# Kernel optimization log

Hardware: AMD Instinct MI355X
Metric: run time of the kernel (lower is better)

## Reference

```python
import jax, jax.numpy as jnp
import numpy as np

B, S = 64, 128
NQ, C = 2000, 128
K, DE, DC = 64, 64, 64


def _glorot(k, shape):
    lim = float(np.sqrt(6.0 / (shape[0] + shape[1])))
    return jax.random.uniform(k, shape, jnp.float32, -lim, lim)


def setup_inputs() -> dict:
    key = jax.random.key(0)
    ks = jax.random.split(key, 16)
    return {
        'question_seq': jax.random.randint(ks[0], (B, S), 0, NQ, dtype=jnp.int32),
        'correctness_seq': jax.random.randint(ks[1], (B, S), 0, 2, dtype=jnp.int32),
        'q_matrix': (jax.random.uniform(ks[2], (NQ, C)) < 0.15).astype(jnp.float32),
        'E_q': jax.random.normal(ks[3], (NQ, DE), jnp.float32) * 0.02,
        'E_c': jax.random.normal(ks[4], (2, DC), jnp.float32) * 0.02,
        'h0': _glorot(ks[5], (C, K)),
        'W1': _glorot(ks[6], (DC + DE, K)), 'b1': jnp.zeros((K,), jnp.float32),
        'W2': _glorot(ks[7], (3 * K, K)), 'b2': jnp.zeros((K,), jnp.float32),
        'W3': _glorot(ks[8], (3 * K, K)), 'b3': jnp.zeros((K,), jnp.float32),
        'W4': _glorot(ks[9], (2 * K, K)), 'b4': jnp.zeros((K,), jnp.float32),
        'Wab': _glorot(ks[10], (K, 1)), 'bab': jnp.zeros((1,), jnp.float32),
        'Wdiff': _glorot(ks[11], (DE, C)), 'bdiff': jnp.zeros((C,), jnp.float32),
        'Wdisc': _glorot(ks[12], (DE, 1)), 'bdisc': jnp.zeros((1,), jnp.float32),
    }


def _forward(question_seq, correctness_seq, q_matrix, E_q, E_c, h0,
             W1, b1, W2, b2, W3, b3, W4, b4,
             Wab, bab, Wdiff, bdiff, Wdisc, bdisc):
    e_emb = E_q[question_seq]                 # [B,S,DE]
    c_emb = E_c[correctness_seq]              # [B,S,DC]
    all_learning = jnp.concatenate([e_emb, c_emb], -1) @ W1 + b1  # [B,S,K]
    q_seq = q_matrix[question_seq]            # [B,S,C]

    h_pre0 = jnp.broadcast_to(h0, (B, C, K))
    h_tilde0 = jnp.einsum('bc,ck->bk', q_seq[:, 0], h0)
    learning0 = jnp.zeros((B, K), jnp.float32)

    xs = (
        jnp.moveaxis(q_seq[:, :-1], 1, 0),        # q_e        [S-1,B,C]
        jnp.moveaxis(all_learning[:, :-1], 1, 0),  # learning   [S-1,B,K]
        jnp.moveaxis(q_seq[:, 1:], 1, 0),         # q_next     [S-1,B,C]
        jnp.moveaxis(e_emb[:, 1:], 1, 0),         # e_next     [S-1,B,DE]
    )

    def step(carry, x):
        h_pre, h_tilde_pre, learning_pre = carry
        q_e, learning, q_next, e_next = x
        cat = jnp.concatenate([learning_pre, learning, h_tilde_pre], -1)  # [B,3K]
        learning_gain = jnp.tanh(cat @ W2 + b2)
        gamma_l = jax.nn.sigmoid(cat @ W3 + b3)
        LG = gamma_l * (learning_gain + 1.0) * 0.5                       # [B,K]
        LG_tilde = q_e[:, :, None] * LG[:, None, :]                      # [B,C,K] rank-1 scatter
        gate_in = jnp.concatenate(
            [h_pre, jnp.broadcast_to(LG[:, None, :], (B, C, K))], -1)    # [B,C,2K]
        gamma_f = jax.nn.sigmoid(gate_in @ W4 + b4)
        h = LG_tilde + gamma_f * h_pre                                   # [B,C,K]
        ability = jax.nn.sigmoid(jnp.squeeze(h @ Wab + bab, -1)) * q_next  # [B,C]
        diff = jax.nn.sigmoid(e_next @ Wdiff + bdiff) * q_next             # [B,C]
        disc = jax.nn.sigmoid(e_next @ Wdisc + bdisc) * 5.0                # [B,1]
        y = jax.nn.sigmoid(jnp.sum(disc * (ability - diff), -1))          # [B]
        h_tilde = jnp.einsum('bc,bck->bk', q_next, h)
        return (h, h_tilde, learning), y

    _, ys = jax.lax.scan(step, (h_pre0, h_tilde0, learning0), xs)  # ys [S-1,B]
    pred = jnp.concatenate([jnp.zeros((B, 1), jnp.float32), ys.T], axis=1)  # [B,S]
    return pred


def reference(question_seq, correctness_seq, q_matrix, E_q, E_c, h0,
              W1, b1, W2, b2, W3, b3, W4, b4,
              Wab, bab, Wdiff, bdiff, Wdisc, bdisc):
    return _forward(question_seq, correctness_seq, q_matrix, E_q, E_c, h0,
                    W1, b1, W2, b2, W3, b3, W4, b4,
                    Wab, bab, Wdiff, bdiff, Wdisc, bdisc)
```

## Files before the change

### kernel.cpp

```cpp
#include <hip/hip_runtime.h>


constexpr int BB = 64, SS = 128, CD = 128;
constexpr int RECF = 136;
constexpr int HP2  = 72;

typedef short bf16x8 __attribute__((ext_vector_type(8)));
typedef float f32x4  __attribute__((ext_vector_type(4)));

#define BAR() asm volatile("s_waitcnt lgkmcnt(0)\ns_barrier" ::: "memory")

__device__ __forceinline__ short f2bf(float x) {
  unsigned u = __builtin_bit_cast(unsigned, x);
  unsigned r = u + 0x7fffu + ((u >> 16) & 1u);
  return (short)(r >> 16);
}
__device__ __forceinline__ unsigned pk2bf(float a, float b) {
  unsigned ua = __builtin_bit_cast(unsigned, a);
  unsigned ub = __builtin_bit_cast(unsigned, b);
  unsigned ra = ua + 0x7fffu + ((ua >> 16) & 1u);
  unsigned rb = ub + 0x7fffu + ((ub >> 16) & 1u);
  return (ra >> 16) | (rb & 0xffff0000u);
}
__device__ __forceinline__ float sigm(float x) {
  return __builtin_amdgcn_rcpf(1.f + __expf(-x));
}
__device__ __forceinline__ bf16x8 pack8(float4 a, float4 b) {
  uint4 u = {pk2bf(a.x, a.y), pk2bf(a.z, a.w), pk2bf(b.x, b.y), pk2bf(b.z, b.w)};
  return __builtin_bit_cast(bf16x8, u);
}
__device__ __forceinline__ void store_bf4(short* p, float a, float b, float c, float d) {
  uint2 v = {pk2bf(a, b), pk2bf(c, d)};
  *(uint2*)p = v;
}

__global__ void pcK(const float* __restrict__ W1, const float* __restrict__ W2,
                    const float* __restrict__ W3, const float* __restrict__ Ec,
                    const float* __restrict__ b1,
                    float* __restrict__ Kws, float* __restrict__ Uws) {
  int m = blockIdx.x, tid = threadIdx.x;
  if (m < 4) {
    const float* src = (m < 2 ? W2 : W3) + (m & 1) * 64 * 64;
    int k = tid & 63, dg = tid >> 6;
    float acc[16];
    #pragma unroll
    for (int i = 0; i < 16; ++i) acc[i] = 0.f;
    for (int j = 0; j < 64; ++j) {
      float w = src[j * 64 + k];
      #pragma unroll
      for (int i = 0; i < 16; ++i) acc[i] += W1[(dg * 16 + i) * 64 + j] * w;
    }
    #pragma unroll
    for (int i = 0; i < 16; ++i) Kws[m * 4096 + (dg * 16 + i) * 64 + k] = acc[i];
  } else {
    __shared__ float alc[2][64];
    if (tid < 128) {
      int cr = tid >> 6, k = tid & 63;
      float s = b1[k];
      for (int d = 0; d < 64; ++d) s += Ec[cr * 64 + d] * W1[(64 + d) * 64 + k];
      alc[cr][k] = s;
    }
    __syncthreads();
    if (tid < 128) {
      int cr = tid >> 6, k = tid & 63;
      float u2a = 0.f, u2b = 0.f, u3a = 0.f, u3b = 0.f;
      for (int j = 0; j < 64; ++j) {
        float a = alc[cr][j];
        u2a += a * W2[j * 64 + k];       u2b += a * W2[(64 + j) * 64 + k];
        u3a += a * W3[j * 64 + k];       u3b += a * W3[(64 + j) * 64 + k];
      }
      Uws[(0 + cr) * 64 + k] = u2a;  Uws[(2 + cr) * 64 + k] = u2b;
      Uws[(4 + cr) * 64 + k] = u3a;  Uws[(6 + cr) * 64 + k] = u3b;
    }
  }
}

__global__ void pcT(const float* __restrict__ Eq, const float* __restrict__ qmat,
                    const float* __restrict__ Wdiff, const float* __restrict__ bdiff,
                    const float* __restrict__ Wdisc, const float* __restrict__ bdisc,
                    const float* __restrict__ Kws,
                    float* __restrict__ T, float* __restrict__ DIFF, float* __restrict__ DISCq) {
  int q0 = blockIdx.x * 8, tid = threadIdx.x;
  __shared__ float e[8][64];
  for (int i = tid; i < 512; i += 256) e[i >> 6][i & 63] = Eq[(q0 + (i >> 6)) * 64 + (i & 63)];
  __syncthreads();
  {
    int m = tid >> 6, k = tid & 63;
    float acc[8] = {0.f, 0.f, 0.f, 0.f, 0.f, 0.f, 0.f, 0.f};
    for (int d = 0; d < 64; ++d) {
      float w = Kws[m * 4096 + d * 64 + k];
      #pragma unroll
      for (int qq = 0; qq < 8; ++qq) acc[qq] += e[qq][d] * w;
    }
    #pragma unroll
    for (int qq = 0; qq < 8; ++qq) T[(q0 + qq) * 256 + m * 64 + k] = acc[qq];
  }
  if (tid < 128) {
    int c = tid;
    float acc[8] = {0.f, 0.f, 0.f, 0.f, 0.f, 0.f, 0.f, 0.f};
    for (int d = 0; d < 64; ++d) {
      float w = Wdiff[d * 128 + c];
      #pragma unroll
      for (int qq = 0; qq < 8; ++qq) acc[qq] += e[qq][d] * w;
    }
    #pragma unroll
    for (int qq = 0; qq < 8; ++qq)
      DIFF[(q0 + qq) * 128 + c] = qmat[(q0 + qq) * 128 + c] * sigm(acc[qq] + bdiff[c]);
  } else if (tid < 136) {
    int qq = tid - 128;
    float s = 0.f;
    for (int d = 0; d < 64; ++d) s += e[qq][d] * Wdisc[d];
    DISCq[q0 + qq] = 5.f * sigm(s + bdisc[0]);
  }
}

__global__ void pcR(const int* __restrict__ qs, const int* __restrict__ cs,
                    const float* __restrict__ qmat,
                    const float* __restrict__ b2, const float* __restrict__ b3,
                    const float* __restrict__ T, const float* __restrict__ Uws,
                    float* __restrict__ REC) {
  int tid = threadIdx.x;
  for (int i = 0; i < 4; ++i) {
    int bs = blockIdx.x * 4 + i;
    int t  = bs & (SS - 1);
    int q_t = qs[bs];
    float* rec = REC + (size_t)bs * RECF;
    if (tid < 64) {
      int k = tid;
      float v2 = b2[k], v3 = b3[k];
      if (t >= 1) {
        int q1 = qs[bs - 1], c1 = cs[bs - 1];
        v2 += T[q1 * 256 + 64 + k]  + Uws[(2 + c1) * 64 + k];
        v3 += T[q1 * 256 + 192 + k] + Uws[(6 + c1) * 64 + k];
      }
      if (t >= 2) {
        int q2 = qs[bs - 2], c2 = cs[bs - 2];
        v2 += T[q2 * 256 + k]       + Uws[(0 + c2) * 64 + k];
        v3 += T[q2 * 256 + 128 + k] + Uws[(4 + c2) * 64 + k];
      }
      int pp = (k & 15) * 4 + (k >> 4);
      rec[pp] = v2; rec[64 + pp] = v3;
    }
    unsigned long long m = __ballot(qmat[q_t * 128 + tid] > 0.5f);
    int wv = tid >> 6, lane = tid & 63;
    if (lane == 0) {
      rec[128 + wv * 2]     = __uint_as_float((unsigned)m);
      rec[128 + wv * 2 + 1] = __uint_as_float((unsigned)(m >> 32));
    }
  }
}

__global__ void pcY(const int* __restrict__ qs, const float* __restrict__ qmat,
                    const float* __restrict__ DIFF, const float* __restrict__ DISCq,
                    const float* __restrict__ YP, const float* __restrict__ bab,
                    float* __restrict__ out) {
  int tid = threadIdx.x, lane = tid & 63, wv = tid >> 6;
  const float bab0 = bab[0];
  __shared__ float red[4][2];
  #pragma unroll
  for (int i = 0; i < 4; ++i) {
    int bs = blockIdx.x * 4 + i;
    int t  = bs & (SS - 1);
    float v = 0.f;
    if (t != 0) {
      int q_t = qs[bs];
      float yp = YP[(size_t)bs * 128 + tid];
      float qn = qmat[q_t * 128 + tid] > 0.5f ? 1.f : 0.f;
      v = sigm(yp + bab0) * qn - DIFF[q_t * 128 + tid];
    }
    v += __shfl_xor(v, 32); v += __shfl_xor(v, 16); v += __shfl_xor(v, 8);
    v += __shfl_xor(v, 4);  v += __shfl_xor(v, 2);  v += __shfl_xor(v, 1);
    if (lane == 0) red[i][wv] = v;
  }
  __syncthreads();
  if (tid < 4) {
    int bs = blockIdx.x * 4 + tid;
    int t  = bs & (SS - 1);
    if (t == 0) out[bs] = 0.f;
    else        out[bs] = sigm(DISCq[qs[bs]] * (red[tid][0] + red[tid][1]));
  }
}

__global__ __launch_bounds__(256, 1) __attribute__((amdgpu_waves_per_eu(1, 1)))
void lpkt_main(
    const float* __restrict__ h0,
    const float* __restrict__ W2, const float* __restrict__ W3,
    const float* __restrict__ W4, const float* __restrict__ b4,
    const float* __restrict__ Wab,
    const float* __restrict__ REC, float* __restrict__ YP) {
  __shared__ __align__(16) short hsb[CD * HP2];
  __shared__ __align__(16) short lgb[4 * 64];
  __shared__ __align__(16) float htbuf[3][64];

  const int b    = blockIdx.x;
  const int tid  = threadIdx.x;
  const int lane = tid & 63;
  const int wv   = tid >> 6;
  const int col  = lane & 15;
  const int quad = lane >> 4;
  const int bS   = b * SS;
  const f32x4 zz = {0.f, 0.f, 0.f, 0.f};

  const float* W4a = W4;
  const float* W4b = W4 + 64 * 64;
  const float* W2c = W2 + 128 * 64;
  const float* W3c = W3 + 128 * 64;

  bf16x8 bw4[4][2], bwb[4][2], bw2[4][2], bw3[4][2], bwab[2];
  float b4r[4];
  #pragma unroll
  for (int nb = 0; nb < 4; ++nb) {
    #pragma unroll
    for (int half = 0; half < 2; ++half)
      #pragma unroll
      for (int j = 0; j < 8; ++j) {
        int p  = half * 32 + quad * 8 + j;
        int ke = (p & 3) * 16 + (p >> 2);
        int kk = ke * 64 + nb * 16 + col;
        bw4[nb][half][j] = f2bf(W4a[kk]);
        bwb[nb][half][j] = f2bf(W4b[kk]);
        bw2[nb][half][j] = f2bf(W2c[kk]);
        bw3[nb][half][j] = f2bf(W3c[kk]);
      }
    b4r[nb] = b4[nb * 16 + col];
  }
  #pragma unroll
  for (int half = 0; half < 2; ++half)
    #pragma unroll
    for (int j = 0; j < 8; ++j) {
      int p  = half * 32 + quad * 8 + j;
      int ke = (p & 3) * 16 + (p >> 2);
      bwab[half][j] = (col == 0) ? f2bf(Wab[ke]) : (short)0;
    }

  float h2[2][4][4];
  #pragma unroll
  for (int mt = 0; mt < 2; ++mt)
    #pragma unroll
    for (int reg = 0; reg < 4; ++reg) {
      int c = 32 * wv + 16 * mt + 4 * quad + reg;
      #pragma unroll
      for (int n = 0; n < 4; ++n) h2[mt][reg][n] = h0[c * 64 + n * 16 + col];
      store_bf4(&hsb[c * HP2 + col * 4],
                h2[mt][reg][0], h2[mt][reg][1], h2[mt][reg][2], h2[mt][reg][3]);
    }
  if (tid < 192) htbuf[tid >> 6][tid & 63] = 0.f;
  __syncthreads();

  float qeR[2][4];
  {
    unsigned qw = __float_as_uint(REC[(size_t)bS * RECF + 128 + wv]);
    float pk[4] = {0.f, 0.f, 0.f, 0.f};
    #pragma unroll
    for (int mt = 0; mt < 2; ++mt) {
      #pragma unroll
      for (int reg = 0; reg < 4; ++reg)
        qeR[mt][reg] = (float)((qw >> (16 * mt + 4 * quad + reg)) & 1u);
      #pragma unroll
      for (int n = 0; n < 4; ++n)
        pk[n] += qeR[mt][0] * h2[mt][0][n] + qeR[mt][1] * h2[mt][1][n]
               + qeR[mt][2] * h2[mt][2][n] + qeR[mt][3] * h2[mt][3][n];
    }
    #pragma unroll
    for (int n = 0; n < 4; ++n) {
      pk[n] += __shfl_xor(pk[n], 16);
      pk[n] += __shfl_xor(pk[n], 32);
    }
    if (quad == 0) {
      #pragma unroll
      for (int n = 0; n < 4; ++n) atomicAdd(&htbuf[1][col * 4 + n], pk[n]);
    }
  }

  unsigned qbw[2];
  qbw[1] = __float_as_uint(REC[(size_t)(bS + 1) * RECF + 128 + wv]);
  qbw[0] = __float_as_uint(REC[(size_t)(bS + 2) * RECF + 128 + wv]);
  float4 pb2[2], pb3[2];
  pb2[1] = *(const float4*)&REC[(size_t)(bS + 1) * RECF + col * 4];
  pb3[1] = *(const float4*)&REC[(size_t)(bS + 1) * RECF + 64 + col * 4];
  pb2[0] = *(const float4*)&REC[(size_t)(bS + 2) * RECF + col * 4];
  pb3[0] = *(const float4*)&REC[(size_t)(bS + 2) * RECF + 64 + col * 4];
  BAR();

  float qnR[2][4];

  for (int t = 1; t < SS; ++t) {
    const float* htb = htbuf[t % 3];
    float4 x0 = *(const float4*)&htb[quad * 8];
    float4 x1 = *(const float4*)&htb[quad * 8 + 4];
    float4 x2 = *(const float4*)&htb[32 + quad * 8];
    float4 x3 = *(const float4*)&htb[32 + quad * 8 + 4];
    bf16x8 af[2][2];
    #pragma unroll
    for (int mt = 0; mt < 2; ++mt) {
      int r = 32 * wv + 16 * mt + col;
      af[mt][0] = *(const bf16x8*)&hsb[r * HP2 + quad * 8];
      af[mt][1] = *(const bf16x8*)&hsb[r * HP2 + 32 + quad * 8];
    }

    unsigned qw = qbw[t & 1];
    #pragma unroll
    for (int mt = 0; mt < 2; ++mt)
      #pragma unroll
      for (int reg = 0; reg < 4; ++reg)
        qnR[mt][reg] = (float)((qw >> (16 * mt + 4 * quad + reg)) & 1u);
    float4 base2 = pb2[t & 1], base3 = pb3[t & 1];
    {
      int tn = (t + 2 < SS) ? t + 2 : SS - 1;
      const float* rn = REC + (size_t)(bS + tn) * RECF;
      qbw[t & 1] = __float_as_uint(rn[128 + wv]);
      pb2[t & 1] = *(const float4*)&rn[col * 4];
      pb3[t & 1] = *(const float4*)&rn[64 + col * 4];
    }

    f32x4 acc[2][4];
    #pragma unroll
    for (int mt = 0; mt < 2; ++mt)
      #pragma unroll
      for (int nb = 0; nb < 4; ++nb) {
        acc[mt][nb] = __builtin_amdgcn_mfma_f32_16x16x32_bf16(af[mt][0], bw4[nb][0], zz, 0, 0, 0);
        acc[mt][nb] = __builtin_amdgcn_mfma_f32_16x16x32_bf16(af[mt][1], bw4[nb][1], acc[mt][nb], 0, 0, 0);
      }
    #pragma unroll
    for (int mt = 0; mt < 2; ++mt) {
      f32x4 ya = __builtin_amdgcn_mfma_f32_16x16x32_bf16(af[mt][0], bwab[0], zz, 0, 0, 0);
      ya = __builtin_amdgcn_mfma_f32_16x16x32_bf16(af[mt][1], bwab[1], ya, 0, 0, 0);
      if (col == 0)
        *(float4*)&YP[((size_t)bS + t - 1) * 128 + 32 * wv + 16 * mt + 4 * quad]
            = make_float4(ya[0], ya[1], ya[2], ya[3]);
    }

    bf16x8 hf0 = pack8(x0, x1), hf1 = pack8(x2, x3);
    float lg[4];
    #pragma unroll
    for (int nb = 0; nb < 4; ++nb) {
      f32x4 a2 = __builtin_amdgcn_mfma_f32_16x16x32_bf16(hf0, bw2[nb][0], zz, 0, 0, 0);
      a2 = __builtin_amdgcn_mfma_f32_16x16x32_bf16(hf1, bw2[nb][1], a2, 0, 0, 0);
      f32x4 a3 = __builtin_amdgcn_mfma_f32_16x16x32_bf16(hf0, bw3[nb][0], zz, 0, 0, 0);
      a3 = __builtin_amdgcn_mfma_f32_16x16x32_bf16(hf1, bw3[nb][1], a3, 0, 0, 0);
      float u2 = a2[0] + ((const float*)&base2)[nb];
      float u3 = a3[0] + ((const float*)&base3)[nb];
      lg[nb] = sigm(u3) * sigm(2.f * u2);
    }
    if (quad == 0) store_bf4(&lgb[wv * 64 + col * 4], lg[0], lg[1], lg[2], lg[3]);
    bf16x8 lf0 = *(const bf16x8*)&lgb[wv * 64 + quad * 8];
    bf16x8 lf1 = *(const bf16x8*)&lgb[wv * 64 + 32 + quad * 8];
    float tvv[4];
    #pragma unroll
    for (int nb = 0; nb < 4; ++nb) {
      f32x4 bb = __builtin_amdgcn_mfma_f32_16x16x32_bf16(lf0, bwb[nb][0], zz, 0, 0, 0);
      bb = __builtin_amdgcn_mfma_f32_16x16x32_bf16(lf1, bwb[nb][1], bb, 0, 0, 0);
      tvv[nb] = bb[0] + b4r[nb];
    }

    #pragma unroll
    for (int mt = 0; mt < 2; ++mt)
      #pragma unroll
      for (int reg = 0; reg < 4; ++reg) {
        int c = 32 * wv + 16 * mt + 4 * quad + reg;
        #pragma unroll
        for (int nb = 0; nb < 4; ++nb) {
          float g = sigm(acc[mt][nb][reg] + tvv[nb]);
          h2[mt][reg][nb] = qeR[mt][reg] * lg[nb] + g * h2[mt][reg][nb];
        }
        store_bf4(&hsb[c * HP2 + col * 4],
                  h2[mt][reg][0], h2[mt][reg][1], h2[mt][reg][2], h2[mt][reg][3]);
      }

    {
      float pk[4] = {0.f, 0.f, 0.f, 0.f};
      #pragma unroll
      for (int mt = 0; mt < 2; ++mt)
        #pragma unroll
        for (int nb = 0; nb < 4; ++nb)
          pk[nb] += qnR[mt][0] * h2[mt][0][nb] + qnR[mt][1] * h2[mt][1][nb]
                  + qnR[mt][2] * h2[mt][2][nb] + qnR[mt][3] * h2[mt][3][nb];
      #pragma unroll
      for (int nb = 0; nb < 4; ++nb) {
        pk[nb] += __shfl_xor(pk[nb], 16);
        pk[nb] += __shfl_xor(pk[nb], 32);
      }
      if (quad == 0) {
        float* dst = htbuf[(t + 1) % 3];
        #pragma unroll
        for (int nb = 0; nb < 4; ++nb) atomicAdd(&dst[col * 4 + nb], pk[nb]);
      }
    }
    if (wv == 3) htbuf[(t + 2) % 3][lane] = 0.f;
    #pragma unroll
    for (int mt = 0; mt < 2; ++mt)
      #pragma unroll
      for (int reg = 0; reg < 4; ++reg) qeR[mt][reg] = qnR[mt][reg];
    BAR();
  }

  #pragma unroll
  for (int mt = 0; mt < 2; ++mt) {
    int r = 32 * wv + 16 * mt + col;
    bf16x8 af0 = *(const bf16x8*)&hsb[r * HP2 + quad * 8];
    bf16x8 af1 = *(const bf16x8*)&hsb[r * HP2 + 32 + quad * 8];
    f32x4 ya = __builtin_amdgcn_mfma_f32_16x16x32_bf16(af0, bwab[0], zz, 0, 0, 0);
    ya = __builtin_amdgcn_mfma_f32_16x16x32_bf16(af1, bwab[1], ya, 0, 0, 0);
    if (col == 0)
      *(float4*)&YP[((size_t)bS + 127) * 128 + 32 * wv + 16 * mt + 4 * quad]
          = make_float4(ya[0], ya[1], ya[2], ya[3]);
  }
}

extern "C" void kernel_launch(void* const* d_in, const int* in_sizes, int n_in,
                              void* d_out, int out_size, void* d_ws, size_t ws_size,
                              hipStream_t stream) {
  const int*   qs    = (const int*)d_in[0];
  const int*   cs    = (const int*)d_in[1];
  const float* qmat  = (const float*)d_in[2];
  const float* Eq    = (const float*)d_in[3];
  const float* Ec    = (const float*)d_in[4];
  const float* h0    = (const float*)d_in[5];
  const float* W1    = (const float*)d_in[6];
  const float* b1    = (const float*)d_in[7];
  const float* W2    = (const float*)d_in[8];
  const float* b2    = (const float*)d_in[9];
  const float* W3    = (const float*)d_in[10];
  const float* b3    = (const float*)d_in[11];
  const float* W4    = (const float*)d_in[12];
  const float* b4    = (const float*)d_in[13];
  const float* Wab   = (const float*)d_in[14];
  const float* bab   = (const float*)d_in[15];
  const float* Wdiff = (const float*)d_in[16];
  const float* bdiff = (const float*)d_in[17];
  const float* Wdisc = (const float*)d_in[18];
  const float* bdisc = (const float*)d_in[19];
  float* out = (float*)d_out;

  float* w = (float*)d_ws;
  float* Kws   = w;
  float* Uws   = Kws + 16384;
  float* T     = Uws + 512;
  float* DIFF  = T + 512000;
  float* DISCq = DIFF + 256000;
  float* REC   = DISCq + 2000;
  float* YP    = REC + (size_t)BB * SS * RECF;

  pcK<<<5, 256, 0, stream>>>(W1, W2, W3, Ec, b1, Kws, Uws);
  pcT<<<250, 256, 0, stream>>>(Eq, qmat, Wdiff, bdiff, Wdisc, bdisc, Kws, T, DIFF, DISCq);
  pcR<<<BB * SS / 4, 128, 0, stream>>>(qs, cs, qmat, b2, b3, T, Uws, REC);
  lpkt_main<<<BB, 256, 0, stream>>>(h0, W2, W3, W4, b4, Wab, REC, YP);
  pcY<<<BB * SS / 4, 128, 0, stream>>>(qs, qmat, DIFF, DISCq, YP, bab, out);
}
```

Before: 429.5 us.

## Restructure recurrent step to compute per-wave partial projections and fold pcK into pcT

The main recurrent kernel now has each wave multiply its partial h_tilde by W2/W3 with MFMA right after the state update. The partials go into double-buffered shared memory and are summed at the start of the next step. This replaces the LDS atomicAdd reduction into a triple-buffered htbuf and moves the W4 gate matmul and ability readout to the end of the step, shortening the critical path between barriers. The small pcK launch is removed: pcT now computes the E_q·W1 product and then W2/W3 per question tile, with block 0 also computing the Uws terms. This saves one launch but repeats W1 work in every block, and the YP indexing is shifted to match the new step ordering.

```diff
diff --git a/kernel.cpp b/kernel.cpp
--- a/kernel.cpp
+++ b/kernel.cpp
@@ -25,34 +25,61 @@
 __device__ __forceinline__ float sigm(float x) {
   return __builtin_amdgcn_rcpf(1.f + __expf(-x));
 }
-__device__ __forceinline__ bf16x8 pack8(float4 a, float4 b) {
-  uint4 u = {pk2bf(a.x, a.y), pk2bf(a.z, a.w), pk2bf(b.x, b.y), pk2bf(b.z, b.w)};
-  return __builtin_bit_cast(bf16x8, u);
-}
 __device__ __forceinline__ void store_bf4(short* p, float a, float b, float c, float d) {
   uint2 v = {pk2bf(a, b), pk2bf(c, d)};
   *(uint2*)p = v;
 }
 
-__global__ void pcK(const float* __restrict__ W1, const float* __restrict__ W2,
+__global__ void pcT(const float* __restrict__ Eq, const float* __restrict__ qmat,
+                    const float* __restrict__ W1, const float* __restrict__ W2,
                     const float* __restrict__ W3, const float* __restrict__ Ec,
                     const float* __restrict__ b1,
-                    float* __restrict__ Kws, float* __restrict__ Uws) {
-  int m = blockIdx.x, tid = threadIdx.x;
-  if (m < 4) {
+                    const float* __restrict__ Wdiff, const float* __restrict__ bdiff,
+                    const float* __restrict__ Wdisc, const float* __restrict__ bdisc,
+                    float* __restrict__ T, float* __restrict__ DIFF,
+                    float* __restrict__ DISCq, float* __restrict__ Uws) {
+  int q0 = blockIdx.x * 8, tid = threadIdx.x;
+  __shared__ float e[8][64], al[8][64];
+  for (int i = tid; i < 512; i += 256) e[i >> 6][i & 63] = Eq[(q0 + (i >> 6)) * 64 + (i & 63)];
+  __syncthreads();
+  for (int i = tid; i < 512; i += 256) {
+    int qq = i >> 6, k = i & 63;
+    float s = 0.f;
+    #pragma unroll 8
+    for (int d = 0; d < 64; ++d) s += e[qq][d] * W1[d * 64 + k];
+    al[qq][k] = s;
+  }
+  __syncthreads();
+  {
+    int m = tid >> 6, k = tid & 63;
     const float* src = (m < 2 ? W2 : W3) + (m & 1) * 64 * 64;
-    int k = tid & 63, dg = tid >> 6;
-    float acc[16];
-    #pragma unroll
-    for (int i = 0; i < 16; ++i) acc[i] = 0.f;
+    float acc[8] = {0.f, 0.f, 0.f, 0.f, 0.f, 0.f, 0.f, 0.f};
     for (int j = 0; j < 64; ++j) {
       float w = src[j * 64 + k];
       #pragma unroll
-      for (int i = 0; i < 16; ++i) acc[i] += W1[(dg * 16 + i) * 64 + j] * w;
-    }
-    #pragma unroll
-    for (int i = 0; i < 16; ++i) Kws[m * 4096 + (dg * 16 + i) * 64 + k] = acc[i];
-  } else {
+      for (int qq = 0; qq < 8; ++qq) acc[qq] += al[qq][j] * w;
+    }
+    #pragma unroll
+    for (int qq = 0; qq < 8; ++qq) T[(q0 + qq) * 256 + m * 64 + k] = acc[qq];
+  }
+  if (tid < 128) {
+    int c = tid;
+    float acc[8] = {0.f, 0.f, 0.f, 0.f, 0.f, 0.f, 0.f, 0.f};
+    for (int d = 0; d < 64; ++d) {
+      float w = Wdiff[d * 128 + c];
+      #pragma unroll
+      for (int qq = 0; qq < 8; ++qq) acc[qq] += e[qq][d] * w;
+    }
+    #pragma unroll
+    for (int qq = 0; qq < 8; ++qq)
+      DIFF[(q0 + qq) * 128 + c] = qmat[(q0 + qq) * 128 + c] * sigm(acc[qq] + bdiff[c]);
+  } else if (tid < 136) {
+    int qq = tid - 128;
+    float s = 0.f;
+    for (int d = 0; d < 64; ++d) s += e[qq][d] * Wdisc[d];
+    DISCq[q0 + qq] = 5.f * sigm(s + bdisc[0]);
+  }
+  if (blockIdx.x == 0) {
     __shared__ float alc[2][64];
     if (tid < 128) {
       int cr = tid >> 6, k = tid & 63;
@@ -72,45 +99,6 @@
       Uws[(0 + cr) * 64 + k] = u2a;  Uws[(2 + cr) * 64 + k] = u2b;
       Uws[(4 + cr) * 64 + k] = u3a;  Uws[(6 + cr) * 64 + k] = u3b;
     }
-  }
-}
-
-__global__ void pcT(const float* __restrict__ Eq, const float* __restrict__ qmat,
-                    const float* __restrict__ Wdiff, const float* __restrict__ bdiff,
-                    const float* __restrict__ Wdisc, const float* __restrict__ bdisc,
-                    const float* __restrict__ Kws,
-                    float* __restrict__ T, float* __restrict__ DIFF, float* __restrict__ DISCq) {
-  int q0 = blockIdx.x * 8, tid = threadIdx.x;
-  __shared__ float e[8][64];
-  for (int i = tid; i < 512; i += 256) e[i >> 6][i & 63] = Eq[(q0 + (i >> 6)) * 64 + (i & 63)];
-  __syncthreads();
-  {
-    int m = tid >> 6, k = tid & 63;
-    float acc[8] = {0.f, 0.f, 0.f, 0.f, 0.f, 0.f, 0.f, 0.f};
-    for (int d = 0; d < 64; ++d) {
-      float w = Kws[m * 4096 + d * 64 + k];
-      #pragma unroll
-      for (int qq = 0; qq < 8; ++qq) acc[qq] += e[qq][d] * w;
-    }
-    #pragma unroll
-    for (int qq = 0; qq < 8; ++qq) T[(q0 + qq) * 256 + m * 64 + k] = acc[qq];
-  }
-  if (tid < 128) {
-    int c = tid;
-    float acc[8] = {0.f, 0.f, 0.f, 0.f, 0.f, 0.f, 0.f, 0.f};
-    for (int d = 0; d < 64; ++d) {
-      float w = Wdiff[d * 128 + c];
-      #pragma unroll
-      for (int qq = 0; qq < 8; ++qq) acc[qq] += e[qq][d] * w;
-    }
-    #pragma unroll
-    for (int qq = 0; qq < 8; ++qq)
-      DIFF[(q0 + qq) * 128 + c] = qmat[(q0 + qq) * 128 + c] * sigm(acc[qq] + bdiff[c]);
-  } else if (tid < 136) {
-    int qq = tid - 128;
-    float s = 0.f;
-    for (int d = 0; d < 64; ++d) s += e[qq][d] * Wdisc[d];
-    DISCq[q0 + qq] = 5.f * sigm(s + bdisc[0]);
   }
 }
 
@@ -190,7 +178,8 @@
     const float* __restrict__ REC, float* __restrict__ YP) {
   __shared__ __align__(16) short hsb[CD * HP2];
   __shared__ __align__(16) short lgb[4 * 64];
-  __shared__ __align__(16) float htbuf[3][64];
+  __shared__ __align__(16) short pkb[4 * 64];
+  __shared__ __align__(16) float up[2][4][2][64];
 
   const int b    = blockIdx.x;
   const int tid  = threadIdx.x;
@@ -244,33 +233,57 @@
       store_bf4(&hsb[c * HP2 + col * 4],
                 h2[mt][reg][0], h2[mt][reg][1], h2[mt][reg][2], h2[mt][reg][3]);
     }
-  if (tid < 192) htbuf[tid >> 6][tid & 63] = 0.f;
-  __syncthreads();
-
-  float qeR[2][4];
+
+  unsigned qe_w = __float_as_uint(REC[(size_t)bS * RECF + 128 + wv]);
   {
-    unsigned qw = __float_as_uint(REC[(size_t)bS * RECF + 128 + wv]);
     float pk[4] = {0.f, 0.f, 0.f, 0.f};
     #pragma unroll
-    for (int mt = 0; mt < 2; ++mt) {
-      #pragma unroll
-      for (int reg = 0; reg < 4; ++reg)
-        qeR[mt][reg] = (float)((qw >> (16 * mt + 4 * quad + reg)) & 1u);
-      #pragma unroll
-      for (int n = 0; n < 4; ++n)
-        pk[n] += qeR[mt][0] * h2[mt][0][n] + qeR[mt][1] * h2[mt][1][n]
-               + qeR[mt][2] * h2[mt][2][n] + qeR[mt][3] * h2[mt][3][n];
-    }
+    for (int mt = 0; mt < 2; ++mt)
+      #pragma unroll
+      for (int reg = 0; reg < 4; ++reg) {
+        float q = (float)((qe_w >> (16 * mt + 4 * quad + reg)) & 1u);
+        #pragma unroll
+        for (int n = 0; n < 4; ++n) pk[n] += q * h2[mt][reg][n];
+      }
     #pragma unroll
     for (int n = 0; n < 4; ++n) {
       pk[n] += __shfl_xor(pk[n], 16);
       pk[n] += __shfl_xor(pk[n], 32);
     }
+    if (quad == 0) store_bf4(&pkb[wv * 64 + col * 4], pk[0], pk[1], pk[2], pk[3]);
+  }
+  bf16x8 pf0 = *(const bf16x8*)&pkb[wv * 64 + quad * 8];
+  bf16x8 pf1 = *(const bf16x8*)&pkb[wv * 64 + 32 + quad * 8];
+  {
+    float v2[4], v3[4];
+    #pragma unroll
+    for (int nb = 0; nb < 4; ++nb) {
+      f32x4 a2 = __builtin_amdgcn_mfma_f32_16x16x32_bf16(pf0, bw2[nb][0], zz, 0, 0, 0);
+      a2 = __builtin_amdgcn_mfma_f32_16x16x32_bf16(pf1, bw2[nb][1], a2, 0, 0, 0);
+      f32x4 a3 = __builtin_amdgcn_mfma_f32_16x16x32_bf16(pf0, bw3[nb][0], zz, 0, 0, 0);
+      a3 = __builtin_amdgcn_mfma_f32_16x16x32_bf16(pf1, bw3[nb][1], a3, 0, 0, 0);
+      v2[nb] = a2[0]; v3[nb] = a3[0];
+    }
     if (quad == 0) {
-      #pragma unroll
-      for (int n = 0; n < 4; ++n) atomicAdd(&htbuf[1][col * 4 + n], pk[n]);
-    }
-  }
+      *(float4*)&up[1][wv][0][col * 4] = make_float4(v2[0], v2[1], v2[2], v2[3]);
+      *(float4*)&up[1][wv][1][col * 4] = make_float4(v3[0], v3[1], v3[2], v3[3]);
+    }
+  }
+  bf16x8 af[2][2];
+  #pragma unroll
+  for (int mt = 0; mt < 2; ++mt) {
+    int r = 32 * wv + 16 * mt + col;
+    af[mt][0] = *(const bf16x8*)&hsb[r * HP2 + quad * 8];
+    af[mt][1] = *(const bf16x8*)&hsb[r * HP2 + 32 + quad * 8];
+  }
+  f32x4 acc[2][4];
+  #pragma unroll
+  for (int mt = 0; mt < 2; ++mt)
+    #pragma unroll
+    for (int nb = 0; nb < 4; ++nb) {
+      acc[mt][nb] = __builtin_amdgcn_mfma_f32_16x16x32_bf16(af[mt][0], bw4[nb][0], zz, 0, 0, 0);
+      acc[mt][nb] = __builtin_amdgcn_mfma_f32_16x16x32_bf16(af[mt][1], bw4[nb][1], acc[mt][nb], 0, 0, 0);
+    }
 
   unsigned qbw[2];
   qbw[1] = __float_as_uint(REC[(size_t)(bS + 1) * RECF + 128 + wv]);
@@ -282,38 +295,100 @@
   pb3[0] = *(const float4*)&REC[(size_t)(bS + 2) * RECF + 64 + col * 4];
   BAR();
 
-  float qnR[2][4];
-
   for (int t = 1; t < SS; ++t) {
-    const float* htb = htbuf[t % 3];
-    float4 x0 = *(const float4*)&htb[quad * 8];
-    float4 x1 = *(const float4*)&htb[quad * 8 + 4];
-    float4 x2 = *(const float4*)&htb[32 + quad * 8];
-    float4 x3 = *(const float4*)&htb[32 + quad * 8 + 4];
-    bf16x8 af[2][2];
+    const int par = t & 1;
+    float4 u2v = pb2[par], u3v = pb3[par];
+    {
+      float4 a0 = *(const float4*)&up[par][0][0][col * 4];
+      float4 a1 = *(const float4*)&up[par][1][0][col * 4];
+      float4 a2 = *(const float4*)&up[par][2][0][col * 4];
+      float4 a3 = *(const float4*)&up[par][3][0][col * 4];
+      float4 c0 = *(const float4*)&up[par][0][1][col * 4];
+      float4 c1 = *(const float4*)&up[par][1][1][col * 4];
+      float4 c2 = *(const float4*)&up[par][2][1][col * 4];
+      float4 c3 = *(const float4*)&up[par][3][1][col * 4];
+      u2v.x += a0.x + a1.x + a2.x + a3.x;  u3v.x += c0.x + c1.x + c2.x + c3.x;
+      u2v.y += a0.y + a1.y + a2.y + a3.y;  u3v.y += c0.y + c1.y + c2.y + c3.y;
+      u2v.z += a0.z + a1.z + a2.z + a3.z;  u3v.z += c0.z + c1.z + c2.z + c3.z;
+      u2v.w += a0.w + a1.w + a2.w + a3.w;  u3v.w += c0.w + c1.w + c2.w + c3.w;
+    }
+    float lg[4];
+    lg[0] = sigm(u3v.x) * sigm(2.f * u2v.x);
+    lg[1] = sigm(u3v.y) * sigm(2.f * u2v.y);
+    lg[2] = sigm(u3v.z) * sigm(2.f * u2v.z);
+    lg[3] = sigm(u3v.w) * sigm(2.f * u2v.w);
+    if (quad == 0) store_bf4(&lgb[wv * 64 + col * 4], lg[0], lg[1], lg[2], lg[3]);
+    unsigned qn_w = qbw[par];
+    {
+      int tn = (t + 2 < SS) ? t + 2 : SS - 1;
+      const float* rn = REC + (size_t)(bS + tn) * RECF;
+      qbw[par] = __float_as_uint(rn[128 + wv]);
+      pb2[par] = *(const float4*)&rn[col * 4];
+      pb3[par] = *(const float4*)&rn[64 + col * 4];
+    }
+    bf16x8 lf0 = *(const bf16x8*)&lgb[wv * 64 + quad * 8];
+    bf16x8 lf1 = *(const bf16x8*)&lgb[wv * 64 + 32 + quad * 8];
+    float tvv[4];
+    #pragma unroll
+    for (int nb = 0; nb < 4; ++nb) {
+      f32x4 bb = __builtin_amdgcn_mfma_f32_16x16x32_bf16(lf0, bwb[nb][0], zz, 0, 0, 0);
+      bb = __builtin_amdgcn_mfma_f32_16x16x32_bf16(lf1, bwb[nb][1], bb, 0, 0, 0);
+      tvv[nb] = bb[0] + b4r[nb];
+    }
+    #pragma unroll
+    for (int mt = 0; mt < 2; ++mt)
+      #pragma unroll
+      for (int reg = 0; reg < 4; ++reg) {
+        int c = 32 * wv + 16 * mt + 4 * quad + reg;
+        float qe = (float)((qe_w >> (16 * mt + 4 * quad + reg)) & 1u);
+        #pragma unroll
+        for (int nb = 0; nb < 4; ++nb) {
+          float g = sigm(acc[mt][nb][reg] + tvv[nb]);
+          h2[mt][reg][nb] = qe * lg[nb] + g * h2[mt][reg][nb];
+        }
+        store_bf4(&hsb[c * HP2 + col * 4],
+                  h2[mt][reg][0], h2[mt][reg][1], h2[mt][reg][2], h2[mt][reg][3]);
+      }
+    {
+      float pk[4] = {0.f, 0.f, 0.f, 0.f};
+      #pragma unroll
+      for (int mt = 0; mt < 2; ++mt)
+        #pragma unroll
+        for (int reg = 0; reg < 4; ++reg) {
+          float q = (float)((qn_w >> (16 * mt + 4 * quad + reg)) & 1u);
+          #pragma unroll
+          for (int n = 0; n < 4; ++n) pk[n] += q * h2[mt][reg][n];
+        }
+      #pragma unroll
+      for (int n = 0; n < 4; ++n) {
+        pk[n] += __shfl_xor(pk[n], 16);
+        pk[n] += __shfl_xor(pk[n], 32);
+      }
+      if (quad == 0) store_bf4(&pkb[wv * 64 + col * 4], pk[0], pk[1], pk[2], pk[3]);
+    }
+    pf0 = *(const bf16x8*)&pkb[wv * 64 + quad * 8];
+    pf1 = *(const bf16x8*)&pkb[wv * 64 + 32 + quad * 8];
+    {
+      float v2[4], v3[4];
+      #pragma unroll
+      for (int nb = 0; nb < 4; ++nb) {
+        f32x4 a2 = __builtin_amdgcn_mfma_f32_16x16x32_bf16(pf0, bw2[nb][0], zz, 0, 0, 0);
+        a2 = __builtin_amdgcn_mfma_f32_16x16x32_bf16(pf1, bw2[nb][1], a2, 0, 0, 0);
+        f32x4 a3 = __builtin_amdgcn_mfma_f32_16x16x32_bf16(pf0, bw3[nb][0], zz, 0, 0, 0);
+        a3 = __builtin_amdgcn_mfma_f32_16x16x32_bf16(pf1, bw3[nb][1], a3, 0, 0, 0);
+        v2[nb] = a2[0]; v3[nb] = a3[0];
+      }
+      if (quad == 0) {
+        *(float4*)&up[par ^ 1][wv][0][col * 4] = make_float4(v2[0], v2[1], v2[2], v2[3]);
+        *(float4*)&up[par ^ 1][wv][1][col * 4] = make_float4(v3[0], v3[1], v3[2], v3[3]);
+      }
+    }
     #pragma unroll
     for (int mt = 0; mt < 2; ++mt) {
       int r = 32 * wv + 16 * mt + col;
       af[mt][0] = *(const bf16x8*)&hsb[r * HP2 + quad * 8];
       af[mt][1] = *(const bf16x8*)&hsb[r * HP2 + 32 + quad * 8];
     }
-
-    unsigned qw = qbw[t & 1];
-    #pragma unroll
-    for (int mt = 0; mt < 2; ++mt)
-      #pragma unroll
-      for (int reg = 0; reg < 4; ++reg)
-        qnR[mt][reg] = (float)((qw >> (16 * mt + 4 * quad + reg)) & 1u);
-    float4 base2 = pb2[t & 1], base3 = pb3[t & 1];
-    {
-      int tn = (t + 2 < SS) ? t + 2 : SS - 1;
-      const float* rn = REC + (size_t)(bS + tn) * RECF;
-      qbw[t & 1] = __float_as_uint(rn[128 + wv]);
-      pb2[t & 1] = *(const float4*)&rn[col * 4];
-      pb3[t & 1] = *(const float4*)&rn[64 + col * 4];
-    }
-
-    f32x4 acc[2][4];
     #pragma unroll
     for (int mt = 0; mt < 2; ++mt)
       #pragma unroll
@@ -326,84 +401,11 @@
       f32x4 ya = __builtin_amdgcn_mfma_f32_16x16x32_bf16(af[mt][0], bwab[0], zz, 0, 0, 0);
       ya = __builtin_amdgcn_mfma_f32_16x16x32_bf16(af[mt][1], bwab[1], ya, 0, 0, 0);
       if (col == 0)
-        *(float4*)&YP[((size_t)bS + t - 1) * 128 + 32 * wv + 16 * mt + 4 * quad]
+        *(float4*)&YP[((size_t)bS + t) * 128 + 32 * wv + 16 * mt + 4 * quad]
             = make_float4(ya[0], ya[1], ya[2], ya[3]);
     }
-
-    bf16x8 hf0 = pack8(x0, x1), hf1 = pack8(x2, x3);
-    float lg[4];
-    #pragma unroll
-    for (int nb = 0; nb < 4; ++nb) {
-      f32x4 a2 = __builtin_amdgcn_mfma_f32_16x16x32_bf16(hf0, bw2[nb][0], zz, 0, 0, 0);
-      a2 = __builtin_amdgcn_mfma_f32_16x16x32_bf16(hf1, bw2[nb][1], a2, 0, 0, 0);
-      f32x4 a3 = __builtin_amdgcn_mfma_f32_16x16x32_bf16(hf0, bw3[nb][0], zz, 0, 0, 0);
-      a3 = __builtin_amdgcn_mfma_f32_16x16x32_bf16(hf1, bw3[nb][1], a3, 0, 0, 0);
-      float u2 = a2[0] + ((const float*)&base2)[nb];
-      float u3 = a3[0] + ((const float*)&base3)[nb];
-      lg[nb] = sigm(u3) * sigm(2.f * u2);
-    }
-    if (quad == 0) store_bf4(&lgb[wv * 64 + col * 4], lg[0], lg[1], lg[2], lg[3]);
-    bf16x8 lf0 = *(const bf16x8*)&lgb[wv * 64 + quad * 8];
-    bf16x8 lf1 = *(const bf16x8*)&lgb[wv * 64 + 32 + quad * 8];
-    float tvv[4];
-    #pragma unroll
-    for (int nb = 0; nb < 4; ++nb) {
-      f32x4 bb = __builtin_amdgcn_mfma_f32_16x16x32_bf16(lf0, bwb[nb][0], zz, 0, 0, 0);
-      bb = __builtin_amdgcn_mfma_f32_16x16x32_bf16(lf1, bwb[nb][1], bb, 0, 0, 0);
-      tvv[nb] = bb[0] + b4r[nb];
-    }
-
-    #pragma unroll
-    for (int mt = 0; mt < 2; ++mt)
-      #pragma unroll
-      for (int reg = 0; reg < 4; ++reg) {
-        int c = 32 * wv + 16 * mt + 4 * quad + reg;
-        #pragma unroll
-        for (int nb = 0; nb < 4; ++nb) {
-          float g = sigm(acc[mt][nb][reg] + tvv[nb]);
-          h2[mt][reg][nb] = qeR[mt][reg] * lg[nb] + g * h2[mt][reg][nb];
-        }
-        store_bf4(&hsb[c * HP2 + col * 4],
-                  h2[mt][reg][0], h2[mt][reg][1], h2[mt][reg][2], h2[mt][reg][3]);
-      }
-
-    {
-      float pk[4] = {0.f, 0.f, 0.f, 0.f};
-      #pragma unroll
-      for (int mt = 0; mt < 2; ++mt)
-        #pragma unroll
-        for (int nb = 0; nb < 4; ++nb)
-          pk[nb] += qnR[mt][0] * h2[mt][0][nb] + qnR[mt][1] * h2[mt][1][nb]
-                  + qnR[mt][2] * h2[mt][2][nb] + qnR[mt][3] * h2[mt][3][nb];
-      #pragma unroll
-      for (int nb = 0; nb < 4; ++nb) {
-        pk[nb] += __shfl_xor(pk[nb], 16);
-        pk[nb] += __shfl_xor(pk[nb], 32);
-      }
-      if (quad == 0) {
-        float* dst = htbuf[(t + 1) % 3];
-        #pragma unroll
-        for (int nb = 0; nb < 4; ++nb) atomicAdd(&dst[col * 4 + nb], pk[nb]);
-      }
-    }
-    if (wv == 3) htbuf[(t + 2) % 3][lane] = 0.f;
-    #pragma unroll
-    for (int mt = 0; mt < 2; ++mt)
-      #pragma unroll
-      for (int reg = 0; reg < 4; ++reg) qeR[mt][reg] = qnR[mt][reg];
+    qe_w = qn_w;
     BAR();
-  }
-
-  #pragma unroll
-  for (int mt = 0; mt < 2; ++mt) {
-    int r = 32 * wv + 16 * mt + col;
-    bf16x8 af0 = *(const bf16x8*)&hsb[r * HP2 + quad * 8];
-    bf16x8 af1 = *(const bf16x8*)&hsb[r * HP2 + 32 + quad * 8];
-    f32x4 ya = __builtin_amdgcn_mfma_f32_16x16x32_bf16(af0, bwab[0], zz, 0, 0, 0);
-    ya = __builtin_amdgcn_mfma_f32_16x16x32_bf16(af1, bwab[1], ya, 0, 0, 0);
-    if (col == 0)
-      *(float4*)&YP[((size_t)bS + 127) * 128 + 32 * wv + 16 * mt + 4 * quad]
-          = make_float4(ya[0], ya[1], ya[2], ya[3]);
   }
 }
 
@@ -433,16 +435,15 @@
   float* out = (float*)d_out;
 
   float* w = (float*)d_ws;
-  float* Kws   = w;
-  float* Uws   = Kws + 16384;
-  float* T     = Uws + 512;
+  float* T     = w;
   float* DIFF  = T + 512000;
   float* DISCq = DIFF + 256000;
-  float* REC   = DISCq + 2000;
+  float* Uws   = DISCq + 2000;
+  float* REC   = Uws + 512;
   float* YP    = REC + (size_t)BB * SS * RECF;
 
-  pcK<<<5, 256, 0, stream>>>(W1, W2, W3, Ec, b1, Kws, Uws);
-  pcT<<<250, 256, 0, stream>>>(Eq, qmat, Wdiff, bdiff, Wdisc, bdisc, Kws, T, DIFF, DISCq);
+  pcT<<<250, 256, 0, stream>>>(Eq, qmat, W1, W2, W3, Ec, b1, Wdiff, bdiff, Wdisc, bdisc,
+                               T, DIFF, DISCq, Uws);
   pcR<<<BB * SS / 4, 128, 0, stream>>>(qs, cs, qmat, b2, b3, T, Uws, REC);
   lpkt_main<<<BB, 256, 0, stream>>>(h0, W2, W3, W4, b4, Wab, REC, YP);
   pcY<<<BB * SS / 4, 128, 0, stream>>>(qs, qmat, DIFF, DISCq, YP, bab, out);
```

Result: faster. 365.1 us (median of 3 runs) (-15.0%).
